# Performance work log

Measured on AMD Instinct MI355X. Metric: run time of the kernel, lower is better.

The kernel has to match this reference:

```python
import jax, jax.numpy as jnp
import numpy as np
import math

C = 512
HEADS = 8
GROUPS = 32
HIDDEN = C * 4
EPS = 1e-5


def group_norm(x, gamma, beta, groups, eps=EPS):
    # x: (b, c, *spatial). Normalize per (sample, group) over (c//g, *spatial).
    b, c = x.shape[0], x.shape[1]
    xg = x.reshape(b, groups, -1)
    mean = xg.mean(axis=-1, keepdims=True)
    var = xg.var(axis=-1, keepdims=True)
    xg = (xg - mean) * jax.lax.rsqrt(var + eps)
    xn = xg.reshape(x.shape)
    shape = (1, c) + (1,) * (x.ndim - 2)
    return xn * gamma.reshape(shape) + beta.reshape(shape)


def setup_inputs() -> dict:
    key = jax.random.key(0)
    ks = jax.random.split(key, 10)
    s = lambda fan_in: 1.0 / math.sqrt(fan_in)
    inp = {
        "x": jax.random.normal(ks[0], (8, C, 32, 32), dtype=jnp.float32),
        "gn1_gamma": jnp.ones((C,), jnp.float32),
        "gn1_beta": jnp.zeros((C,), jnp.float32),
        "qkv_w": jax.random.uniform(ks[1], (3 * C, C), jnp.float32, -s(C), s(C)),
        "qkv_b": jax.random.uniform(ks[2], (3 * C,), jnp.float32, -s(C), s(C)),
        "out_w": jax.random.uniform(ks[3], (C, C), jnp.float32, -s(C), s(C)),
        "out_b": jax.random.uniform(ks[4], (C,), jnp.float32, -s(C), s(C)),
        "gn2_gamma": jnp.ones((C,), jnp.float32),
        "gn2_beta": jnp.zeros((C,), jnp.float32),
        "mlp1_w": jax.random.uniform(ks[5], (2 * HIDDEN, C), jnp.float32, -s(C), s(C)),
        "mlp2_w": jax.random.uniform(ks[6], (C, HIDDEN), jnp.float32, -s(HIDDEN), s(HIDDEN)),
    }
    return inp


def reference(x, gn1_gamma, gn1_beta, qkv_w, qkv_b, out_w, out_b,
              gn2_gamma, gn2_beta, mlp1_w, mlp2_w):
    b, c, h, w = x.shape
    n = h * w
    head_dim = c // HEADS
    x_norm = group_norm(x, gn1_gamma, gn1_beta, GROUPS).reshape(b, c, n)
    # 1x1 conv1d == channel matmul
    qkv = jnp.einsum('oc,bcn->bon', qkv_w, x_norm) + qkv_b[None, :, None]
    q, k, v = jnp.split(qkv, 3, axis=1)
    split_heads = lambda t: t.reshape(b, HEADS, head_dim, n).transpose(0, 1, 3, 2)  # b h n d
    q, k, v = split_heads(q), split_heads(k), split_heads(v)
    attn = jnp.einsum('bhnd,bhmd->bhnm', q, k) / math.sqrt(head_dim)
    attn = jax.nn.softmax(attn, axis=-1)  # internally max-stabilized
    x_attn = jnp.einsum('bhnm,bhmd->bhnd', attn, v)
    x_attn = x_attn.transpose(0, 1, 3, 2).reshape(b, c, n)  # b (h d) n
    x_attn = jnp.einsum('oc,bcn->bon', out_w, x_attn) + out_b[None, :, None]
    x_attn = group_norm(x_attn, gn2_gamma, gn2_beta, GROUPS)
    x_attn = x_attn.transpose(0, 2, 1)  # b n c
    hgate = x_attn @ mlp1_w.T  # b n 2*hidden
    h1, gate = jnp.split(hgate, 2, axis=-1)
    x_attn = jax.nn.silu(h1) * gate
    x_attn = x_attn @ mlp2_w.T  # b n c
    x_attn = x_attn.transpose(0, 2, 1).reshape(b, c, h, w)
    return x + x_attn
```

## Files before the change

### kernel.cpp

```cpp
#include <hip/hip_runtime.h>

typedef unsigned short ushort_t;
typedef __bf16 bf16x8 __attribute__((ext_vector_type(8)));
typedef float f32x4 __attribute__((ext_vector_type(4)));
typedef unsigned short u16x8 __attribute__((ext_vector_type(8)));
typedef unsigned short u16x4 __attribute__((ext_vector_type(4)));
typedef unsigned int __attribute__((address_space(1))) as1_uint;
typedef unsigned int __attribute__((address_space(3))) as3_uint;

#define DEV __device__ __forceinline__

DEV float bf2f(ushort_t u) { union { float f; unsigned i; } c; c.i = (unsigned)u << 16; return c.f; }
DEV ushort_t f2bf(float f) {
  union { float f; unsigned i; } c; c.f = f;
  return (ushort_t)((c.i + 0x7FFFu + ((c.i >> 16) & 1u)) >> 16);
}

DEV f32x4 mfma16(bf16x8 a, bf16x8 b, f32x4 c) {
  return __builtin_amdgcn_mfma_f32_16x16x32_bf16(a, b, c, 0, 0, 0);
}

DEV void g2lds16(const void* g, void* l) {
  __builtin_amdgcn_global_load_lds((as1_uint*)g, (as3_uint*)l, 16, 0, 0);
}

__global__ __launch_bounds__(256) void cvt_all(const float* __restrict__ w0, const float* __restrict__ w1,
                                               const float* __restrict__ w2, const float* __restrict__ w3,
                                               ushort_t* __restrict__ o0, ushort_t* __restrict__ o1,
                                               ushort_t* __restrict__ o2, ushort_t* __restrict__ o3) {
  int i = blockIdx.x * 256 + threadIdx.x;
  const float* src; ushort_t* dst; int base;
  if (i < 196608)      { src = w0; dst = o0; base = 0; }
  else if (i < 262144) { src = w1; dst = o1; base = 196608; }
  else if (i < 786432) { src = w2; dst = o2; base = 262144; }
  else                 { src = w3; dst = o3; base = 786432; }
  int j = i - base;
  float4 v = ((const float4*)src)[j];
  u16x4 o;
  o[0] = f2bf(v.x); o[1] = f2bf(v.y); o[2] = f2bf(v.z); o[3] = f2bf(v.w);
  ((u16x4*)dst)[j] = o;
}

__global__ __launch_bounds__(256) void gn_stats_cn(const float* __restrict__ x, float* __restrict__ st) {
  int b = blockIdx.x >> 5, g = blockIdx.x & 31;
  const float4* base = (const float4*)(x + ((size_t)b * 512 + g * 16) * 1024);
  float s = 0.f, sq = 0.f;
  for (int i = threadIdx.x; i < 4096; i += 256) {
    float4 v = base[i];
    s += v.x + v.y + v.z + v.w;
    sq += v.x * v.x + v.y * v.y + v.z * v.z + v.w * v.w;
  }
  #pragma unroll
  for (int mk = 1; mk < 64; mk <<= 1) { s += __shfl_xor(s, mk); sq += __shfl_xor(sq, mk); }
  __shared__ float red[8];
  if ((threadIdx.x & 63) == 0) { red[(threadIdx.x >> 6) * 2] = s; red[(threadIdx.x >> 6) * 2 + 1] = sq; }
  __syncthreads();
  if (threadIdx.x == 0) {
    s = red[0] + red[2] + red[4] + red[6];
    sq = red[1] + red[3] + red[5] + red[7];
    float mean = s * (1.f / 16384.f);
    float var = sq * (1.f / 16384.f) - mean * mean;
    st[blockIdx.x * 2] = mean;
    st[blockIdx.x * 2 + 1] = rsqrtf(var + 1e-5f);
  }
}

__global__ __launch_bounds__(256) void gn_stats_nc(const ushort_t* __restrict__ OP, float* __restrict__ st) {
  int b = blockIdx.x >> 5, g = blockIdx.x & 31;
  float s = 0.f, sq = 0.f;
  for (int jj = threadIdx.x; jj < 2048; jj += 256) {
    int n = jj >> 1, c8 = (jj & 1) * 8;
    u16x8 v = *(const u16x8*)(OP + (size_t)(b * 1024 + n) * 512 + g * 16 + c8);
    #pragma unroll
    for (int t = 0; t < 8; ++t) { float f = bf2f(v[t]); s += f; sq += f * f; }
  }
  #pragma unroll
  for (int mk = 1; mk < 64; mk <<= 1) { s += __shfl_xor(s, mk); sq += __shfl_xor(sq, mk); }
  __shared__ float red[8];
  if ((threadIdx.x & 63) == 0) { red[(threadIdx.x >> 6) * 2] = s; red[(threadIdx.x >> 6) * 2 + 1] = sq; }
  __syncthreads();
  if (threadIdx.x == 0) {
    s = red[0] + red[2] + red[4] + red[6];
    sq = red[1] + red[3] + red[5] + red[7];
    float mean = s * (1.f / 16384.f);
    float var = sq * (1.f / 16384.f) - mean * mean;
    st[blockIdx.x * 2] = mean;
    st[blockIdx.x * 2 + 1] = rsqrtf(var + 1e-5f);
  }
}

__global__ __launch_bounds__(256) void gn1_norm_t(const float* __restrict__ x, const float* __restrict__ st,
                                                  const float* __restrict__ gamma, const float* __restrict__ beta,
                                                  ushort_t* __restrict__ XN) {
  __shared__ float tile[64][65];
  int b = blockIdx.z, c0 = blockIdx.y * 64, n0 = blockIdx.x * 64;
  int tx = threadIdx.x & 63, ty = threadIdx.x >> 6;
  for (int i = ty; i < 64; i += 4) {
    int c = c0 + i;
    float mean = st[(b * 32 + (c >> 4)) * 2], rstd = st[(b * 32 + (c >> 4)) * 2 + 1];
    float v = x[((size_t)b * 512 + c) * 1024 + n0 + tx];
    tile[i][tx] = (v - mean) * rstd * gamma[c] + beta[c];
  }
  __syncthreads();
  for (int j = ty; j < 64; j += 4)
    XN[(size_t)(b * 1024 + n0 + j) * 512 + c0 + tx] = f2bf(tile[tx][j]);
}

__global__ __launch_bounds__(256) void transpose_v(const ushort_t* __restrict__ QKVT, ushort_t* __restrict__ VT) {
  __shared__ ushort_t tile[64][65];
  int b = blockIdx.z, c0 = blockIdx.y * 64, n0 = blockIdx.x * 64;
  int tx = threadIdx.x & 63, ty = threadIdx.x >> 6;
  for (int j = ty; j < 64; j += 4)
    tile[j][tx] = QKVT[(size_t)(b * 1024 + n0 + j) * 1536 + 1024 + c0 + tx];
  __syncthreads();
  for (int i = ty; i < 64; i += 4)
    VT[((size_t)b * 512 + c0 + i) * 1024 + n0 + tx] = tile[tx][i];
}

__global__ __launch_bounds__(256) void gn2_norm(const ushort_t* __restrict__ OP, const float* __restrict__ st,
                                                const float* __restrict__ gamma, const float* __restrict__ beta,
                                                ushort_t* __restrict__ XN2) {
  size_t idx = ((size_t)blockIdx.x * 256 + threadIdx.x) * 8;
  int c0 = (int)(idx & 511);
  int gi = (int)(idx >> 9);
  int b = gi >> 10;
  int g = c0 >> 4;
  float mean = st[(b * 32 + g) * 2], rstd = st[(b * 32 + g) * 2 + 1];
  u16x8 v = *(const u16x8*)(OP + idx);
  u16x8 o;
  #pragma unroll
  for (int t = 0; t < 8; ++t) {
    int c = c0 + t;
    o[t] = f2bf((bf2f(v[t]) - mean) * rstd * gamma[c] + beta[c]);
  }
  *(u16x8*)(XN2 + idx) = o;
}

template <int EPI, int NJ>
__global__ __launch_bounds__(256) void gemm_bt(const ushort_t* __restrict__ A, int lda,
                                               const ushort_t* __restrict__ B, int ldb,
                                               const float* __restrict__ bias,
                                               void* __restrict__ Out, int ldo, int K,
                                               const float* __restrict__ resid) {
  constexpr int BN = NJ * 32;
  __shared__ __align__(16) ushort_t As[128 * 64];
  __shared__ __align__(16) ushort_t Bs[BN * 64];
  const int tid = threadIdx.x;
  const int lane = tid & 63, wave = tid >> 6;
  const int l15 = lane & 15, l4 = lane >> 4;
  const int m0 = blockIdx.y * 128, n0 = blockIdx.x * BN;
  const int wr = (wave >> 1) * 64, wc = (wave & 1) * (NJ * 16);
  f32x4 acc[4][NJ] = {};
  for (int k0 = 0; k0 < K; k0 += 64) {
    #pragma unroll
    for (int p = 0; p < 4; ++p) {
      int s = p * 256 + wave * 64 + lane;
      int row = s >> 3, c8 = (s & 7) * 8;
      g2lds16(A + (size_t)(m0 + row) * lda + k0 + c8, (char*)As + (p * 256 + wave * 64) * 16);
    }
    #pragma unroll
    for (int p = 0; p < NJ; ++p) {
      int s = p * 256 + wave * 64 + lane;
      int row = s >> 3, c8 = (s & 7) * 8;
      g2lds16(B + (size_t)(n0 + row) * ldb + k0 + c8, (char*)Bs + (p * 256 + wave * 64) * 16);
    }
    __syncthreads();
    #pragma unroll
    for (int ks = 0; ks < 2; ++ks) {
      bf16x8 af[4], bfr[NJ];
      #pragma unroll
      for (int i = 0; i < 4; ++i)
        af[i] = *(const bf16x8*)(As + (wr + i * 16 + l15) * 64 + ks * 32 + l4 * 8);
      #pragma unroll
      for (int j = 0; j < NJ; ++j)
        bfr[j] = *(const bf16x8*)(Bs + (wc + j * 16 + l15) * 64 + ks * 32 + l4 * 8);
      #pragma unroll
      for (int i = 0; i < 4; ++i)
        #pragma unroll
        for (int j = 0; j < NJ; ++j)
          acc[i][j] = mfma16(af[i], bfr[j], acc[i][j]);
    }
    __syncthreads();
  }
  #pragma unroll
  for (int i = 0; i < 4; ++i) {
    #pragma unroll
    for (int j = 0; j < NJ; ++j) {
      int row = m0 + wr + i * 16 + l4 * 4;
      int col = n0 + wc + j * 16 + l15;
      if constexpr (EPI == 0) {
        float bv = bias ? bias[col] : 0.f;
        ushort_t* o = (ushort_t*)Out;
        #pragma unroll
        for (int r = 0; r < 4; ++r)
          o[(size_t)(row + r) * ldo + col] = f2bf(acc[i][j][r] + bv);
      } else {
        int bb = row >> 10, n = row & 1023;
        size_t idx = ((size_t)bb * 512 + col) * 1024 + n;
        float4 rv = *(const float4*)(resid + idx);
        float4 ov = make_float4(acc[i][j][0] + rv.x, acc[i][j][1] + rv.y,
                                acc[i][j][2] + rv.z, acc[i][j][3] + rv.w);
        *(float4*)((float*)Out + idx) = ov;
      }
    }
  }
}

__global__ __launch_bounds__(256) void gemm_mlp1(const ushort_t* __restrict__ A,
                                                 const ushort_t* __restrict__ B1,
                                                 const ushort_t* __restrict__ B2,
                                                 ushort_t* __restrict__ Out) {
  __shared__ __align__(16) ushort_t As[128 * 64];
  __shared__ __align__(16) ushort_t B1s[64 * 64];
  __shared__ __align__(16) ushort_t B2s[64 * 64];
  const int tid = threadIdx.x;
  const int lane = tid & 63, wave = tid >> 6;
  const int l15 = lane & 15, l4 = lane >> 4;
  const int m0 = blockIdx.y * 128, n0 = blockIdx.x * 64;
  const int wr = (wave >> 1) * 64, wc = (wave & 1) * 32;
  f32x4 acc1[4][2] = {};
  f32x4 acc2[4][2] = {};
  for (int k0 = 0; k0 < 512; k0 += 64) {
    #pragma unroll
    for (int p = 0; p < 4; ++p) {
      int s = p * 256 + wave * 64 + lane;
      int row = s >> 3, c8 = (s & 7) * 8;
      g2lds16(A + (size_t)(m0 + row) * 512 + k0 + c8, (char*)As + (p * 256 + wave * 64) * 16);
    }
    #pragma unroll
    for (int p = 0; p < 2; ++p) {
      int s = p * 256 + wave * 64 + lane;
      int row = s >> 3, c8 = (s & 7) * 8;
      g2lds16(B1 + (size_t)(n0 + row) * 512 + k0 + c8, (char*)B1s + (p * 256 + wave * 64) * 16);
      g2lds16(B2 + (size_t)(n0 + row) * 512 + k0 + c8, (char*)B2s + (p * 256 + wave * 64) * 16);
    }
    __syncthreads();
    #pragma unroll
    for (int ks = 0; ks < 2; ++ks) {
      bf16x8 af[4], b1f[2], b2f[2];
      #pragma unroll
      for (int i = 0; i < 4; ++i)
        af[i] = *(const bf16x8*)(As + (wr + i * 16 + l15) * 64 + ks * 32 + l4 * 8);
      #pragma unroll
      for (int j = 0; j < 2; ++j) {
        b1f[j] = *(const bf16x8*)(B1s + (wc + j * 16 + l15) * 64 + ks * 32 + l4 * 8);
        b2f[j] = *(const bf16x8*)(B2s + (wc + j * 16 + l15) * 64 + ks * 32 + l4 * 8);
      }
      #pragma unroll
      for (int i = 0; i < 4; ++i)
        #pragma unroll
        for (int j = 0; j < 2; ++j) {
          acc1[i][j] = mfma16(af[i], b1f[j], acc1[i][j]);
          acc2[i][j] = mfma16(af[i], b2f[j], acc2[i][j]);
        }
    }
    __syncthreads();
  }
  #pragma unroll
  for (int i = 0; i < 4; ++i) {
    #pragma unroll
    for (int j = 0; j < 2; ++j) {
      int row = m0 + wr + i * 16 + l4 * 4;
      int col = n0 + wc + j * 16 + l15;
      #pragma unroll
      for (int r = 0; r < 4; ++r) {
        float h1 = acc1[i][j][r];
        float sg = h1 / (1.f + __expf(-h1));
        Out[(size_t)(row + r) * 2048 + col] = f2bf(sg * acc2[i][j][r]);
      }
    }
  }
}

__global__ __launch_bounds__(256) void attn_kernel(const ushort_t* __restrict__ QKVT,
                                                   const ushort_t* __restrict__ VT,
                                                   ushort_t* __restrict__ AT) {
  __shared__ __align__(16) ushort_t Kt[64 * 64];
  __shared__ __align__(16) ushort_t Vt[64 * 64];
  __shared__ __align__(16) ushort_t Pl[4][32 * 64];
  const int tid = threadIdx.x, lane = tid & 63, wave = tid >> 6;
  const int l15 = lane & 15, l4 = lane >> 4;
  const int bh = blockIdx.x, b = bh >> 3, h = bh & 7;
  const int q0 = blockIdx.y * 128;
  bf16x8 qf[2][2];
  #pragma unroll
  for (int i = 0; i < 2; ++i)
    #pragma unroll
    for (int ks = 0; ks < 2; ++ks)
      qf[i][ks] = *(const bf16x8*)(QKVT + (size_t)(b * 1024 + q0 + wave * 32 + i * 16 + l15) * 1536 +
                                   h * 64 + ks * 32 + l4 * 8);
  f32x4 acc_o[2][4] = {};
  f32x4 mst[2], lst[2];
  #pragma unroll
  for (int i = 0; i < 2; ++i)
    #pragma unroll
    for (int r = 0; r < 4; ++r) { mst[i][r] = -1e30f; lst[i][r] = 0.f; }
  const float scale = 0.125f;
  for (int m0 = 0; m0 < 1024; m0 += 64) {
    #pragma unroll
    for (int p = 0; p < 2; ++p) {
      int s = p * 256 + wave * 64 + lane;
      int row = s >> 3, c8 = ((s & 7) ^ (row & 7)) * 8;
      g2lds16(QKVT + (size_t)(b * 1024 + m0 + row) * 1536 + 512 + h * 64 + c8,
              (char*)Kt + (p * 256 + wave * 64) * 16);
      g2lds16(VT + ((size_t)b * 512 + h * 64 + row) * 1024 + m0 + c8,
              (char*)Vt + (p * 256 + wave * 64) * 16);
    }
    __syncthreads();
    f32x4 accs[2][4] = {};
    #pragma unroll
    for (int ks = 0; ks < 2; ++ks) {
      bf16x8 kf[4];
      #pragma unroll
      for (int j = 0; j < 4; ++j)
        kf[j] = *(const bf16x8*)(Kt + (j * 16 + l15) * 64 + (((ks * 4 + l4) ^ (l15 & 7)) << 3));
      #pragma unroll
      for (int i = 0; i < 2; ++i)
        #pragma unroll
        for (int j = 0; j < 4; ++j)
          accs[i][j] = mfma16(qf[i][ks], kf[j], accs[i][j]);
    }
    #pragma unroll
    for (int i = 0; i < 2; ++i) {
      float tm[4], al[4], rs[4];
      #pragma unroll
      for (int r = 0; r < 4; ++r) {
        float t = accs[i][0][r];
        #pragma unroll
        for (int j = 1; j < 4; ++j) t = fmaxf(t, accs[i][j][r]);
        tm[r] = t * scale;
      }
      #pragma unroll
      for (int mk = 1; mk < 16; mk <<= 1)
        #pragma unroll
        for (int r = 0; r < 4; ++r)
          tm[r] = fmaxf(tm[r], __shfl_xor(tm[r], mk));
      #pragma unroll
      for (int r = 0; r < 4; ++r) {
        float mn = fmaxf(mst[i][r], tm[r]);
        al[r] = __expf(mst[i][r] - mn);
        mst[i][r] = mn;
        rs[r] = 0.f;
      }
      #pragma unroll
      for (int j = 0; j < 4; ++j)
        #pragma unroll
        for (int r = 0; r < 4; ++r) {
          float pv = __expf(accs[i][j][r] * scale - mst[i][r]);
          accs[i][j][r] = pv;
          rs[r] += pv;
        }
      #pragma unroll
      for (int mk = 1; mk < 16; mk <<= 1)
        #pragma unroll
        for (int r = 0; r < 4; ++r)
          rs[r] += __shfl_xor(rs[r], mk);
      #pragma unroll
      for (int r = 0; r < 4; ++r) lst[i][r] = lst[i][r] * al[r] + rs[r];
      #pragma unroll
      for (int jd = 0; jd < 4; ++jd)
        #pragma unroll
        for (int r = 0; r < 4; ++r) acc_o[i][jd][r] *= al[r];
      #pragma unroll
      for (int j = 0; j < 4; ++j)
        #pragma unroll
        for (int r = 0; r < 4; ++r) {
          int prow = i * 16 + l4 * 4 + r, pcol = j * 16 + l15;
          Pl[wave][prow * 64 + ((((pcol >> 3) ^ (prow & 7)) << 3) | (pcol & 7))] =
              f2bf(accs[i][j][r]);
        }
    }
    #pragma unroll
    for (int km = 0; km < 2; ++km) {
      bf16x8 pf[2];
      #pragma unroll
      for (int i = 0; i < 2; ++i)
        pf[i] = *(const bf16x8*)(&Pl[wave][(i * 16 + l15) * 64 + (((km * 4 + l4) ^ (l15 & 7)) << 3)]);
      #pragma unroll
      for (int jd = 0; jd < 4; ++jd) {
        bf16x8 vf = *(const bf16x8*)(Vt + (jd * 16 + l15) * 64 + (((km * 4 + l4) ^ (l15 & 7)) << 3));
        #pragma unroll
        for (int i = 0; i < 2; ++i)
          acc_o[i][jd] = mfma16(pf[i], vf, acc_o[i][jd]);
      }
    }
    __syncthreads();
  }
  #pragma unroll
  for (int i = 0; i < 2; ++i) {
    float inv[4];
    #pragma unroll
    for (int r = 0; r < 4; ++r) inv[r] = 1.f / lst[i][r];
    #pragma unroll
    for (int jd = 0; jd < 4; ++jd)
      #pragma unroll
      for (int r = 0; r < 4; ++r)
        AT[(size_t)(b * 1024 + q0 + wave * 32 + i * 16 + l4 * 4 + r) * 512 + h * 64 + jd * 16 + l15] =
            f2bf(acc_o[i][jd][r] * inv[r]);
  }
}

extern "C" void kernel_launch(void* const* d_in, const int* in_sizes, int n_in,
                              void* d_out, int out_size, void* d_ws, size_t ws_size,
                              hipStream_t stream) {
  const float* x    = (const float*)d_in[0];
  const float* g1   = (const float*)d_in[1];
  const float* b1   = (const float*)d_in[2];
  const float* qkvw = (const float*)d_in[3];
  const float* qkvb = (const float*)d_in[4];
  const float* outw = (const float*)d_in[5];
  const float* outb = (const float*)d_in[6];
  const float* g2   = (const float*)d_in[7];
  const float* b2   = (const float*)d_in[8];
  const float* m1w  = (const float*)d_in[9];
  const float* m2w  = (const float*)d_in[10];

  char* ws = (char*)d_ws;
  const size_t MB = 1ull << 20;
  ushort_t* XN   = (ushort_t*)(ws + 0);
  ushort_t* QKVT = (ushort_t*)(ws + 8 * MB);
  ushort_t* VT   = (ushort_t*)(ws + 32 * MB);
  ushort_t* AT   = (ushort_t*)(ws + 40 * MB);
  ushort_t* OP   = (ushort_t*)(ws + 48 * MB);
  ushort_t* XN2  = (ushort_t*)(ws + 0);
  ushort_t* HID  = (ushort_t*)(ws + 8 * MB);
  ushort_t* WQ   = (ushort_t*)(ws + 88 * MB);
  ushort_t* WO   = (ushort_t*)(ws + 90 * MB);
  ushort_t* WM1  = (ushort_t*)(ws + 91 * MB);
  ushort_t* WM2  = (ushort_t*)(ws + 96 * MB);
  float*    ST1  = (float*)(ws + 99 * MB);
  float*    ST2  = (float*)(ws + 99 * MB + 4096);

  cvt_all<<<4096, 256, 0, stream>>>(qkvw, outw, m1w, m2w, WQ, WO, WM1, WM2);

  gn_stats_cn<<<256, 256, 0, stream>>>(x, ST1);
  gn1_norm_t<<<dim3(16, 8, 8), 256, 0, stream>>>(x, ST1, g1, b1, XN);

  gemm_bt<0, 2><<<dim3(24, 64), 256, 0, stream>>>(XN, 512, WQ, 512, qkvb, QKVT, 1536, 512, nullptr);
  transpose_v<<<dim3(16, 8, 8), 256, 0, stream>>>(QKVT, VT);
  attn_kernel<<<dim3(64, 8), 256, 0, stream>>>(QKVT, VT, AT);

  gemm_bt<0, 2><<<dim3(8, 64), 256, 0, stream>>>(AT, 512, WO, 512, outb, OP, 512, 512, nullptr);
  gn_stats_nc<<<256, 256, 0, stream>>>(OP, ST2);
  gn2_norm<<<2048, 256, 0, stream>>>(OP, ST2, g2, b2, XN2);

  gemm_mlp1<<<dim3(32, 64), 256, 0, stream>>>(XN2, WM1, WM1 + 2048 * 512, HID);

  gemm_bt<1, 2><<<dim3(8, 64), 256, 0, stream>>>(HID, 2048, WM2, 2048, nullptr, d_out, 0, 2048, x);
}
```

Measured before the change: 323.1 us.

## Double-buffer GEMM and attention loads, add XCD swizzle, widen attention blocks

Adds LDS double buffering to the out-projection and MLP2 GEMMs and to the attention K/V tiles, so global-to-LDS loads for the next tile overlap the MFMA work on the current one. Remaps workgroup IDs so that neighbouring tiles land on the same XCD, aiming for better L2 reuse. Restructures attention into 512-thread blocks with 16 query rows per wave, uses s_setprio around MFMA sections, and halves per-wave register state. The cost is more LDS per block and some risk of lower occupancy or extra register pressure.

```diff
diff --git a/kernel.cpp b/kernel.cpp
--- a/kernel.cpp
+++ b/kernel.cpp
@@ -22,6 +22,16 @@
 
 DEV void g2lds16(const void* g, void* l) {
   __builtin_amdgcn_global_load_lds((as1_uint*)g, (as3_uint*)l, 16, 0, 0);
+}
+
+DEV void xcd_swz(int gx, int gy, int& bx, int& by) {
+  int nwg = gx * gy;
+  int wg = by * gx + bx;
+  int q = nwg >> 3, r = nwg & 7;
+  int xcd = wg & 7, idx = wg >> 3;
+  int swz = (xcd < r ? xcd * (q + 1) : r * (q + 1) + (xcd - r) * q) + idx;
+  bx = swz % gx;
+  by = swz / gx;
 }
 
 __global__ __launch_bounds__(256) void cvt_all(const float* __restrict__ w0, const float* __restrict__ w1,
@@ -136,52 +146,79 @@
   *(u16x8*)(XN2 + idx) = o;
 }
 
-template <int EPI, int NJ>
+template <int EPI, bool DBUF>
 __global__ __launch_bounds__(256) void gemm_bt(const ushort_t* __restrict__ A, int lda,
                                                const ushort_t* __restrict__ B, int ldb,
                                                const float* __restrict__ bias,
                                                void* __restrict__ Out, int ldo, int K,
                                                const float* __restrict__ resid) {
+  constexpr int NJ = 2;
   constexpr int BN = NJ * 32;
-  __shared__ __align__(16) ushort_t As[128 * 64];
-  __shared__ __align__(16) ushort_t Bs[BN * 64];
+  constexpr int NB = DBUF ? 2 : 1;
+  __shared__ __align__(16) ushort_t As[NB][128 * 64];
+  __shared__ __align__(16) ushort_t Bs[NB][BN * 64];
   const int tid = threadIdx.x;
   const int lane = tid & 63, wave = tid >> 6;
   const int l15 = lane & 15, l4 = lane >> 4;
-  const int m0 = blockIdx.y * 128, n0 = blockIdx.x * BN;
+  int bx = blockIdx.x, by = blockIdx.y;
+  xcd_swz(gridDim.x, gridDim.y, bx, by);
+  const int m0 = by * 128, n0 = bx * BN;
   const int wr = (wave >> 1) * 64, wc = (wave & 1) * (NJ * 16);
   f32x4 acc[4][NJ] = {};
-  for (int k0 = 0; k0 < K; k0 += 64) {
+
+  auto stage = [&](int bufi, int kk) {
     #pragma unroll
     for (int p = 0; p < 4; ++p) {
       int s = p * 256 + wave * 64 + lane;
       int row = s >> 3, c8 = (s & 7) * 8;
-      g2lds16(A + (size_t)(m0 + row) * lda + k0 + c8, (char*)As + (p * 256 + wave * 64) * 16);
+      g2lds16(A + (size_t)(m0 + row) * lda + kk + c8, (char*)As[bufi] + (p * 256 + wave * 64) * 16);
     }
     #pragma unroll
     for (int p = 0; p < NJ; ++p) {
       int s = p * 256 + wave * 64 + lane;
       int row = s >> 3, c8 = (s & 7) * 8;
-      g2lds16(B + (size_t)(n0 + row) * ldb + k0 + c8, (char*)Bs + (p * 256 + wave * 64) * 16);
-    }
-    __syncthreads();
+      g2lds16(B + (size_t)(n0 + row) * ldb + kk + c8, (char*)Bs[bufi] + (p * 256 + wave * 64) * 16);
+    }
+  };
+  auto compute = [&](int bufi) {
+    const ushort_t* Asb = As[bufi];
+    const ushort_t* Bsb = Bs[bufi];
     #pragma unroll
     for (int ks = 0; ks < 2; ++ks) {
       bf16x8 af[4], bfr[NJ];
       #pragma unroll
       for (int i = 0; i < 4; ++i)
-        af[i] = *(const bf16x8*)(As + (wr + i * 16 + l15) * 64 + ks * 32 + l4 * 8);
+        af[i] = *(const bf16x8*)(Asb + (wr + i * 16 + l15) * 64 + ks * 32 + l4 * 8);
       #pragma unroll
       for (int j = 0; j < NJ; ++j)
-        bfr[j] = *(const bf16x8*)(Bs + (wc + j * 16 + l15) * 64 + ks * 32 + l4 * 8);
+        bfr[j] = *(const bf16x8*)(Bsb + (wc + j * 16 + l15) * 64 + ks * 32 + l4 * 8);
       #pragma unroll
       for (int i = 0; i < 4; ++i)
         #pragma unroll
         for (int j = 0; j < NJ; ++j)
           acc[i][j] = mfma16(af[i], bfr[j], acc[i][j]);
     }
+  };
+
+  if constexpr (DBUF) {
+    stage(0, 0);
     __syncthreads();
-  }
+    int cur = 0;
+    for (int k0 = 0; k0 < K; k0 += 64) {
+      if (k0 + 64 < K) stage(cur ^ 1, k0 + 64);
+      compute(cur);
+      __syncthreads();
+      cur ^= 1;
+    }
+  } else {
+    for (int k0 = 0; k0 < K; k0 += 64) {
+      stage(0, k0);
+      __syncthreads();
+      compute(0);
+      __syncthreads();
+    }
+  }
+
   #pragma unroll
   for (int i = 0; i < 4; ++i) {
     #pragma unroll
@@ -216,7 +253,9 @@
   const int tid = threadIdx.x;
   const int lane = tid & 63, wave = tid >> 6;
   const int l15 = lane & 15, l4 = lane >> 4;
-  const int m0 = blockIdx.y * 128, n0 = blockIdx.x * 64;
+  int bx = blockIdx.x, by = blockIdx.y;
+  xcd_swz(gridDim.x, gridDim.y, bx, by);
+  const int m0 = by * 128, n0 = bx * 64;
   const int wr = (wave >> 1) * 64, wc = (wave & 1) * 32;
   f32x4 acc1[4][2] = {};
   f32x4 acc2[4][2] = {};
@@ -272,132 +311,122 @@
   }
 }
 
-__global__ __launch_bounds__(256) void attn_kernel(const ushort_t* __restrict__ QKVT,
-                                                   const ushort_t* __restrict__ VT,
-                                                   ushort_t* __restrict__ AT) {
-  __shared__ __align__(16) ushort_t Kt[64 * 64];
-  __shared__ __align__(16) ushort_t Vt[64 * 64];
-  __shared__ __align__(16) ushort_t Pl[4][32 * 64];
+__global__ __launch_bounds__(512, 4) void attn_kernel(const ushort_t* __restrict__ QKVT,
+                                                      const ushort_t* __restrict__ VT,
+                                                      ushort_t* __restrict__ AT) {
+  __shared__ __align__(16) ushort_t Kt[2][64 * 64];
+  __shared__ __align__(16) ushort_t Vt[2][64 * 64];
+  __shared__ __align__(16) ushort_t Pl[8][16 * 64];
   const int tid = threadIdx.x, lane = tid & 63, wave = tid >> 6;
   const int l15 = lane & 15, l4 = lane >> 4;
-  const int bh = blockIdx.x, b = bh >> 3, h = bh & 7;
-  const int q0 = blockIdx.y * 128;
-  bf16x8 qf[2][2];
-  #pragma unroll
-  for (int i = 0; i < 2; ++i)
-    #pragma unroll
-    for (int ks = 0; ks < 2; ++ks)
-      qf[i][ks] = *(const bf16x8*)(QKVT + (size_t)(b * 1024 + q0 + wave * 32 + i * 16 + l15) * 1536 +
-                                   h * 64 + ks * 32 + l4 * 8);
-  f32x4 acc_o[2][4] = {};
-  f32x4 mst[2], lst[2];
-  #pragma unroll
-  for (int i = 0; i < 2; ++i)
-    #pragma unroll
-    for (int r = 0; r < 4; ++r) { mst[i][r] = -1e30f; lst[i][r] = 0.f; }
+  int bx = blockIdx.x, by = blockIdx.y;
+  xcd_swz(gridDim.x, gridDim.y, bx, by);
+  const int b = bx >> 3, h = bx & 7;
+  const int qr0 = by * 128 + wave * 16;
+  bf16x8 qf[2];
+  #pragma unroll
+  for (int ks = 0; ks < 2; ++ks)
+    qf[ks] = *(const bf16x8*)(QKVT + (size_t)(b * 1024 + qr0 + l15) * 1536 + h * 64 + ks * 32 + l4 * 8);
+  f32x4 acc_o[4] = {};
+  float mst[4], lst[4];
+  #pragma unroll
+  for (int r = 0; r < 4; ++r) { mst[r] = -1e30f; lst[r] = 0.f; }
   const float scale = 0.125f;
-  for (int m0 = 0; m0 < 1024; m0 += 64) {
-    #pragma unroll
-    for (int p = 0; p < 2; ++p) {
-      int s = p * 256 + wave * 64 + lane;
-      int row = s >> 3, c8 = ((s & 7) ^ (row & 7)) * 8;
-      g2lds16(QKVT + (size_t)(b * 1024 + m0 + row) * 1536 + 512 + h * 64 + c8,
-              (char*)Kt + (p * 256 + wave * 64) * 16);
-      g2lds16(VT + ((size_t)b * 512 + h * 64 + row) * 1024 + m0 + c8,
-              (char*)Vt + (p * 256 + wave * 64) * 16);
-    }
+
+  auto stage = [&](int bufi, int m0) {
+    int s = tid;
+    int row = s >> 3, c8 = ((s & 7) ^ (row & 7)) * 8;
+    g2lds16(QKVT + (size_t)(b * 1024 + m0 + row) * 1536 + 512 + h * 64 + c8,
+            (char*)Kt[bufi] + (wave * 64) * 16);
+    g2lds16(VT + ((size_t)b * 512 + h * 64 + row) * 1024 + m0 + c8,
+            (char*)Vt[bufi] + (wave * 64) * 16);
+  };
+
+  stage(0, 0);
+  __syncthreads();
+  int cur = 0;
+  for (int t = 0; t < 16; ++t) {
+    if (t < 15) stage(cur ^ 1, (t + 1) * 64);
+    const ushort_t* Ktb = Kt[cur];
+    const ushort_t* Vtb = Vt[cur];
+    f32x4 accs[4] = {};
+    __builtin_amdgcn_s_setprio(1);
+    #pragma unroll
+    for (int ks = 0; ks < 2; ++ks) {
+      #pragma unroll
+      for (int j = 0; j < 4; ++j) {
+        bf16x8 kf = *(const bf16x8*)(Ktb + (j * 16 + l15) * 64 + (((ks * 4 + l4) ^ (l15 & 7)) << 3));
+        accs[j] = mfma16(qf[ks], kf, accs[j]);
+      }
+    }
+    __builtin_amdgcn_s_setprio(0);
+    float tm[4], al[4], rs[4];
+    #pragma unroll
+    for (int r = 0; r < 4; ++r) {
+      float t0 = fmaxf(fmaxf(accs[0][r], accs[1][r]), fmaxf(accs[2][r], accs[3][r]));
+      tm[r] = t0 * scale;
+    }
+    #pragma unroll
+    for (int mk = 1; mk < 16; mk <<= 1)
+      #pragma unroll
+      for (int r = 0; r < 4; ++r)
+        tm[r] = fmaxf(tm[r], __shfl_xor(tm[r], mk));
+    #pragma unroll
+    for (int r = 0; r < 4; ++r) {
+      float mn = fmaxf(mst[r], tm[r]);
+      al[r] = __expf(mst[r] - mn);
+      mst[r] = mn;
+      rs[r] = 0.f;
+    }
+    #pragma unroll
+    for (int j = 0; j < 4; ++j)
+      #pragma unroll
+      for (int r = 0; r < 4; ++r) {
+        float pv = __expf(accs[j][r] * scale - mst[r]);
+        accs[j][r] = pv;
+        rs[r] += pv;
+      }
+    #pragma unroll
+    for (int mk = 1; mk < 16; mk <<= 1)
+      #pragma unroll
+      for (int r = 0; r < 4; ++r)
+        rs[r] += __shfl_xor(rs[r], mk);
+    #pragma unroll
+    for (int r = 0; r < 4; ++r) lst[r] = lst[r] * al[r] + rs[r];
+    #pragma unroll
+    for (int jd = 0; jd < 4; ++jd)
+      #pragma unroll
+      for (int r = 0; r < 4; ++r) acc_o[jd][r] *= al[r];
+    #pragma unroll
+    for (int j = 0; j < 4; ++j)
+      #pragma unroll
+      for (int r = 0; r < 4; ++r) {
+        int prow = l4 * 4 + r, pcol = j * 16 + l15;
+        Pl[wave][prow * 64 + ((((pcol >> 3) ^ (prow & 7)) << 3) | (pcol & 7))] = f2bf(accs[j][r]);
+      }
+    __builtin_amdgcn_s_setprio(1);
+    #pragma unroll
+    for (int km = 0; km < 2; ++km) {
+      bf16x8 pf = *(const bf16x8*)(&Pl[wave][l15 * 64 + (((km * 4 + l4) ^ (l15 & 7)) << 3)]);
+      #pragma unroll
+      for (int jd = 0; jd < 4; ++jd) {
+        bf16x8 vf = *(const bf16x8*)(Vtb + (jd * 16 + l15) * 64 + (((km * 4 + l4) ^ (l15 & 7)) << 3));
+        acc_o[jd] = mfma16(pf, vf, acc_o[jd]);
+      }
+    }
+    __builtin_amdgcn_s_setprio(0);
     __syncthreads();
-    f32x4 accs[2][4] = {};
-    #pragma unroll
-    for (int ks = 0; ks < 2; ++ks) {
-      bf16x8 kf[4];
-      #pragma unroll
-      for (int j = 0; j < 4; ++j)
-        kf[j] = *(const bf16x8*)(Kt + (j * 16 + l15) * 64 + (((ks * 4 + l4) ^ (l15 & 7)) << 3));
-      #pragma unroll
-      for (int i = 0; i < 2; ++i)
-        #pragma unroll
-        for (int j = 0; j < 4; ++j)
-          accs[i][j] = mfma16(qf[i][ks], kf[j], accs[i][j]);
-    }
-    #pragma unroll
-    for (int i = 0; i < 2; ++i) {
-      float tm[4], al[4], rs[4];
-      #pragma unroll
-      for (int r = 0; r < 4; ++r) {
-        float t = accs[i][0][r];
-        #pragma unroll
-        for (int j = 1; j < 4; ++j) t = fmaxf(t, accs[i][j][r]);
-        tm[r] = t * scale;
-      }
-      #pragma unroll
-      for (int mk = 1; mk < 16; mk <<= 1)
-        #pragma unroll
-        for (int r = 0; r < 4; ++r)
-          tm[r] = fmaxf(tm[r], __shfl_xor(tm[r], mk));
-      #pragma unroll
-      for (int r = 0; r < 4; ++r) {
-        float mn = fmaxf(mst[i][r], tm[r]);
-        al[r] = __expf(mst[i][r] - mn);
-        mst[i][r] = mn;
-        rs[r] = 0.f;
-      }
-      #pragma unroll
-      for (int j = 0; j < 4; ++j)
-        #pragma unroll
-        for (int r = 0; r < 4; ++r) {
-          float pv = __expf(accs[i][j][r] * scale - mst[i][r]);
-          accs[i][j][r] = pv;
-          rs[r] += pv;
-        }
-      #pragma unroll
-      for (int mk = 1; mk < 16; mk <<= 1)
-        #pragma unroll
-        for (int r = 0; r < 4; ++r)
-          rs[r] += __shfl_xor(rs[r], mk);
-      #pragma unroll
-      for (int r = 0; r < 4; ++r) lst[i][r] = lst[i][r] * al[r] + rs[r];
-      #pragma unroll
-      for (int jd = 0; jd < 4; ++jd)
-        #pragma unroll
-        for (int r = 0; r < 4; ++r) acc_o[i][jd][r] *= al[r];
-      #pragma unroll
-      for (int j = 0; j < 4; ++j)
-        #pragma unroll
-        for (int r = 0; r < 4; ++r) {
-          int prow = i * 16 + l4 * 4 + r, pcol = j * 16 + l15;
-          Pl[wave][prow * 64 + ((((pcol >> 3) ^ (prow & 7)) << 3) | (pcol & 7))] =
-              f2bf(accs[i][j][r]);
-        }
-    }
-    #pragma unroll
-    for (int km = 0; km < 2; ++km) {
-      bf16x8 pf[2];
-      #pragma unroll
-      for (int i = 0; i < 2; ++i)
-        pf[i] = *(const bf16x8*)(&Pl[wave][(i * 16 + l15) * 64 + (((km * 4 + l4) ^ (l15 & 7)) << 3)]);
-      #pragma unroll
-      for (int jd = 0; jd < 4; ++jd) {
-        bf16x8 vf = *(const bf16x8*)(Vt + (jd * 16 + l15) * 64 + (((km * 4 + l4) ^ (l15 & 7)) << 3));
-        #pragma unroll
-        for (int i = 0; i < 2; ++i)
-          acc_o[i][jd] = mfma16(pf[i], vf, acc_o[i][jd]);
-      }
-    }
-    __syncthreads();
-  }
-  #pragma unroll
-  for (int i = 0; i < 2; ++i) {
-    float inv[4];
-    #pragma unroll
-    for (int r = 0; r < 4; ++r) inv[r] = 1.f / lst[i][r];
-    #pragma unroll
-    for (int jd = 0; jd < 4; ++jd)
-      #pragma unroll
-      for (int r = 0; r < 4; ++r)
-        AT[(size_t)(b * 1024 + q0 + wave * 32 + i * 16 + l4 * 4 + r) * 512 + h * 64 + jd * 16 + l15] =
-            f2bf(acc_o[i][jd][r] * inv[r]);
-  }
+    cur ^= 1;
+  }
+  float inv[4];
+  #pragma unroll
+  for (int r = 0; r < 4; ++r) inv[r] = 1.f / lst[r];
+  #pragma unroll
+  for (int jd = 0; jd < 4; ++jd)
+    #pragma unroll
+    for (int r = 0; r < 4; ++r)
+      AT[(size_t)(b * 1024 + qr0 + l4 * 4 + r) * 512 + h * 64 + jd * 16 + l15] =
+          f2bf(acc_o[jd][r] * inv[r]);
 }
 
 extern "C" void kernel_launch(void* const* d_in, const int* in_sizes, int n_in,
@@ -436,15 +465,15 @@
   gn_stats_cn<<<256, 256, 0, stream>>>(x, ST1);
   gn1_norm_t<<<dim3(16, 8, 8), 256, 0, stream>>>(x, ST1, g1, b1, XN);
 
-  gemm_bt<0, 2><<<dim3(24, 64), 256, 0, stream>>>(XN, 512, WQ, 512, qkvb, QKVT, 1536, 512, nullptr);
+  gemm_bt<0, false><<<dim3(24, 64), 256, 0, stream>>>(XN, 512, WQ, 512, qkvb, QKVT, 1536, 512, nullptr);
   transpose_v<<<dim3(16, 8, 8), 256, 0, stream>>>(QKVT, VT);
-  attn_kernel<<<dim3(64, 8), 256, 0, stream>>>(QKVT, VT, AT);
-
-  gemm_bt<0, 2><<<dim3(8, 64), 256, 0, stream>>>(AT, 512, WO, 512, outb, OP, 512, 512, nullptr);
+  attn_kernel<<<dim3(64, 8), 512, 0, stream>>>(QKVT, VT, AT);
+
+  gemm_bt<0, true><<<dim3(8, 64), 256, 0, stream>>>(AT, 512, WO, 512, outb, OP, 512, 512, nullptr);
   gn_stats_nc<<<256, 256, 0, stream>>>(OP, ST2);
   gn2_norm<<<2048, 256, 0, stream>>>(OP, ST2, g2, b2, XN2);
 
   gemm_mlp1<<<dim3(32, 64), 256, 0, stream>>>(XN2, WM1, WM1 + 2048 * 512, HID);
 
-  gemm_bt<1, 2><<<dim3(8, 64), 256, 0, stream>>>(HID, 2048, WM2, 2048, nullptr, d_out, 0, 2048, x);
-}
+  gemm_bt<1, true><<<dim3(8, 64), 256, 0, stream>>>(HID, 2048, WM2, 2048, nullptr, d_out, 0, 2048, x);
+}
```

New measurement: 327.9 us. No clear change (+1.5%).
